# Kernel tuning notes

Measured on AMD Instinct MI355X. Metric: run time of the kernel, lower is better.

The kernel has to match this reference:

```python
import jax, jax.numpy as jnp
import numpy as np

JIT = 1e-4
LOG2PI = float(np.log(2.0 * np.pi))
BETA = 1e5
LOC_RADIUS = 5.0


def gaspari_cohn(radius, D):
    i = np.arange(D)
    dist = np.minimum(np.abs(i[:, None] - i[None, :]), D - np.abs(i[:, None] - i[None, :])).astype(np.float64)
    z = dist / radius
    zs = np.maximum(z, 1e-12)
    g1 = 1.0 - 5.0 / 3 * z**2 + 5.0 / 8 * z**3 + 0.5 * z**4 - 0.25 * z**5
    g2 = 4.0 - 5.0 * z + 5.0 / 3 * z**2 + 5.0 / 8 * z**3 - 0.5 * z**4 + 1.0 / 12 * z**5 - 2.0 / (3.0 * zs)
    return np.where(z < 1.0, g1, np.where(z < 2.0, g2, 0.0)).astype(np.float32)


def sq_dist(x, z):
    # x: [..., n, d], z: [..., m, d] (broadcastable)
    x2 = jnp.sum(x * x, -1)[..., :, None]
    z2 = jnp.sum(z * z, -1)[..., None, :]
    d2 = x2 + z2 - 2.0 * jnp.matmul(x, jnp.swapaxes(z, -1, -2))
    return jnp.maximum(d2, 0.0)


def setup_inputs():
    key = jax.random.key(0)
    ks = jax.random.split(key, 12)
    D, dy, M, N, B, T = 32, 32, 128, 128, 8, 48
    ips = jax.random.normal(ks[0], (D, M, D), dtype=jnp.float32)
    H = jnp.eye(dy, D, dtype=jnp.float32)
    lengthscale = jnp.full((D,), 2.0, dtype=jnp.float32)
    outputscale = jnp.ones((D,), dtype=jnp.float32)
    q_mu = 0.1 * jax.random.normal(ks[1], (D, M), dtype=jnp.float32)
    q_L = jnp.tril(0.02 * jax.random.normal(ks[2], (D, M, M), dtype=jnp.float32), -1) + 0.1 * jnp.eye(M, dtype=jnp.float32)[None]
    q_noise = jnp.full((D,), 0.05**2, dtype=jnp.float32)
    r_noise = jnp.full((dy,), 0.1**2, dtype=jnp.float32)
    x0 = jax.random.normal(ks[3], (N, D, B, D), dtype=jnp.float32)
    y = 0.5 * jax.random.normal(ks[4], (B, T, dy), dtype=jnp.float32)
    eps_u = jax.random.normal(ks[5], (N, D, M), dtype=jnp.float32)
    eps_f = jax.random.normal(ks[6], (T, N, D, B), dtype=jnp.float32)
    eps_q = jax.random.normal(ks[7], (T, B, N, D), dtype=jnp.float32)
    eps_r = jax.random.normal(ks[8], (T, B, N, dy), dtype=jnp.float32)
    return {"ips": ips, "H": H, "lengthscale": lengthscale, "outputscale": outputscale,
            "q_mu": q_mu, "q_L": q_L, "q_noise": q_noise, "r_noise": r_noise,
            "x0": x0, "y": y, "eps_u": eps_u, "eps_f": eps_f, "eps_q": eps_q, "eps_r": eps_r}


def _forward(ips, H, lengthscale, outputscale, q_mu, q_L, q_noise, r_noise, x0, y, eps_u, eps_f, eps_q, eps_r):
    N, D, B, _ = x0.shape
    M = ips.shape[1]
    dy = y.shape[-1]
    taper = jnp.asarray(gaspari_cohn(LOC_RADIUS, D))
    ls = lengthscale[:, None, None]
    osc = outputscale[:, None, None]
    zs = ips / ls  # [D, M, D]
    Kzz = osc * jnp.exp(-0.5 * sq_dist(zs, zs)) + JIT * jnp.eye(M, dtype=x0.dtype)  # [D,M,M]
    # U ~ q(u): consistent sampling of inducing outputs per ensemble member
    U = q_mu[None] + jnp.einsum('dmk,ndk->ndm', q_L, eps_u)                 # [N,D,M]
    A = jnp.linalg.solve(Kzz[None], U[..., None])[..., 0]                    # Kzz^{-1} u, [N,D,M]
    # KL(q(u) || N(0, Kzz)) summed over tasks
    Lzz = jnp.linalg.cholesky(Kzz)
    Sq = q_L @ jnp.swapaxes(q_L, -1, -2)
    trace = jnp.sum(jnp.diagonal(jnp.linalg.solve(Kzz, Sq), axis1=-2, axis2=-1))
    mah = jnp.sum(q_mu * jnp.linalg.solve(Kzz, q_mu[..., None])[..., 0])
    logdetK = 2.0 * jnp.sum(jnp.log(jnp.diagonal(Lzz, axis1=-2, axis2=-1)))
    logdetS = 2.0 * jnp.sum(jnp.log(jnp.abs(jnp.diagonal(q_L, axis1=-2, axis2=-1))))
    kl = 0.5 * (trace + mah - D * M + logdetK - logdetS)

    q_sd = jnp.sqrt(q_noise)
    r_sd = jnp.sqrt(r_noise)
    R = jnp.diag(r_noise)
    Ht = H.T
    eyeB = jnp.eye(B, dtype=x0.dtype)

    def step(carry, inp):
        x_prev, ll = carry
        y_t, ef, eq, er = inp
        # ---- GP prediction (conditioned on sampled U) ----
        xq = x_prev / lengthscale[None, :, None, None]                       # [N,D,B,D]
        Kxz = outputscale[None, :, None, None] * jnp.exp(-0.5 * sq_dist(xq, zs[None]))  # [N,D,B,M]
        Kxx = outputscale[None, :, None, None] * jnp.exp(-0.5 * sq_dist(xq, xq))        # [N,D,B,B]
        mean = jnp.einsum('ndbm,ndm->ndb', Kxz, A)
        V = jnp.linalg.solve(Kzz[None], jnp.swapaxes(Kxz, -1, -2))           # [N,D,M,B]
        cov = Kxx - jnp.matmul(Kxz, V) + JIT * eyeB
        Lc = jnp.linalg.cholesky(cov)
        f = mean + jnp.einsum('ndbc,ndc->ndb', Lc, ef)                       # rsample, [N,D,B]
        X = jnp.transpose(f, (2, 0, 1))                                      # [B,N,D]
        X = X + eq * q_sd                                                    # + chol(Q) noise
        Xm = jnp.mean(X, axis=-2, keepdims=True)                             # [B,1,D]
        Xc = X - Xm
        P = taper * (jnp.swapaxes(Xc, -1, -2) @ Xc) / (N - 1)                # localized cov [B,D,D]
        # ---- EnKF update ----
        S = H @ P @ Ht + R                                                   # [B,dy,dy]
        Ls = jnp.linalg.cholesky(S)
        resid = y_t - (Xm @ Ht)[:, 0]                                        # [B,dy]
        alpha = jnp.linalg.solve(S, resid[..., None])[..., 0]
        logdetS_t = 2.0 * jnp.sum(jnp.log(jnp.diagonal(Ls, axis1=-2, axis2=-1)), axis=-1)
        ll_t = -0.5 * jnp.sum(dy * LOG2PI + logdetS_t + jnp.sum(resid * alpha, -1))
        PHt = P @ Ht
        K = jnp.swapaxes(jnp.linalg.solve(S, jnp.swapaxes(PHt, -1, -2)), -1, -2)  # [B,D,dy]
        y_pert = y_t[:, None, :] + er * r_sd
        X_post = X + (y_pert - X @ Ht) @ jnp.swapaxes(K, -1, -2)
        Xm_post = jnp.mean(X_post, axis=-2)                                  # [B,D]
        P_post = P - K @ (H @ P)
        x_next = jnp.broadcast_to(Xm_post[None, None], (N, D, B, D))         # ensemble reset to post. mean
        return (x_next, ll + ll_t), (Xm_post, jnp.diagonal(P_post, axis1=-2, axis2=-1))

    ys = jnp.swapaxes(y, 0, 1)  # [T,B,dy]
    (x_final, ll), (fm, fv) = jax.lax.scan(step, (x0, jnp.asarray(0.0, x0.dtype)), (ys, eps_f, eps_q, eps_r))
    filtered_mean = jnp.swapaxes(fm, 0, 1)  # [B,T,D]
    filtered_var = jnp.swapaxes(fv, 0, 1)   # [B,T,D]
    elbo = ll - kl / BETA
    return elbo, x_final, filtered_mean, filtered_var


def reference(ips, H, lengthscale, outputscale, q_mu, q_L, q_noise, r_noise, x0, y, eps_u, eps_f, eps_q, eps_r):
    return _forward(ips, H, lengthscale, outputscale, q_mu, q_L, q_noise, r_noise, x0, y, eps_u, eps_f, eps_q, eps_r)
```

## Files before the change

### kernel.cpp

```cpp
#include <hip/hip_runtime.h>

#define JITF 1e-4f
#define LOG2PIF 1.8378770664093454f

#define WZSM   0
#define WZS2   131072
#define WKINV  135168
#define WA     659456
#define WXW    1708032
#define WXM    1740800
#define WLLB   1741056
#define WKLD   1741088
#define WCNT   1741248
#define OFM 1048577
#define OFV 1060865

__device__ __forceinline__ float dot4f(const float4 a, const float4 b) {
  return fmaf(a.x, b.x, fmaf(a.y, b.y, fmaf(a.z, b.z, a.w * b.w)));
}
__device__ __forceinline__ float4 f4_fma(const float4 a, const float s, const float4 c) {
  return make_float4(fmaf(a.x,s,c.x), fmaf(a.y,s,c.y), fmaf(a.z,s,c.z), fmaf(a.w,s,c.w));
}
__device__ __forceinline__ float4 f4_axpby(const float a, const float4 x, const float b, const float4 y) {
  return make_float4(fmaf(a,x.x,b*y.x), fmaf(a,x.y,b*y.y), fmaf(a,x.z,b*y.z), fmaf(a,x.w,b*y.w));
}
__device__ __forceinline__ float aloadf(const float* p) {
  return __hip_atomic_load((float*)p, __ATOMIC_RELAXED, __HIP_MEMORY_SCOPE_AGENT);
}
__device__ __forceinline__ void astoref(float* p, float v) {
  __hip_atomic_store(p, v, __ATOMIC_RELAXED, __HIP_MEMORY_SCOPE_AGENT);
}
__device__ __forceinline__ unsigned long long aloadu(const unsigned long long* p) {
  return __hip_atomic_load((unsigned long long*)p, __ATOMIC_RELAXED, __HIP_MEMORY_SCOPE_AGENT);
}
__device__ __forceinline__ void pollge(const int* p, int target) {
  while (__hip_atomic_load((int*)p, __ATOMIC_RELAXED, __HIP_MEMORY_SCOPE_AGENT) < target)
    __builtin_amdgcn_s_sleep(1);
}
__device__ __forceinline__ void gsignal(int* p, int val, int tid) {
  __syncthreads();
  if (tid == 0) __hip_atomic_store(p, val, __ATOMIC_RELEASE, __HIP_MEMORY_SCOPE_AGENT);
}

__global__ __launch_bounds__(1024) void k_sweep(
    const float* __restrict__ ips, const float* __restrict__ ls, const float* __restrict__ osc,
    const float* __restrict__ qL, const float* __restrict__ qmu,
    float* __restrict__ zsMg, float* __restrict__ zs2g,
    float* __restrict__ Kinvg, float* __restrict__ kld, int* cnt)
{
  __shared__ float sm[40200];
  float* cur   = sm;
  float* qLs   = sm + 16896;
  float* zsM   = sm + 33792;
  float* rowP0 = sm + 38400;
  float* rowP1 = sm + 38532;
  float* colP0 = sm + 38664;
  float* colP1 = sm + 38792;
  float* qms   = sm + 38920;
  float* zs2   = sm + 39048;
  float* red   = sm + 39176;
  float4* cur4 = (float4*)cur;
  const float4* zsM4 = (const float4*)zsM;
  float4* rowP04 = (float4*)rowP0;
  float4* rowP14 = (float4*)rowP1;
  const int d = blockIdx.x, tid = threadIdx.x;
  const float invl = 1.0f / ls[d], oscd = osc[d];

  if (blockIdx.x == 0) { for (int l = tid; l < 640; l += 1024) cnt[l] = 0; }

  for (int l = tid; l < 4096; l += 1024) {
    int m = l >> 5, k = l & 31;
    zsM[m*36+k] = ips[(d*128+m)*32+k] * invl;
  }
  for (int l = tid; l < 16384; l += 1024)
    qLs[(l>>7)*132 + (l&127)] = qL[d*16384 + l];
  if (tid < 128) qms[tid] = qmu[d*128+tid];
  __syncthreads();
  if (tid < 128) {
    float s = 0.f;
#pragma unroll
    for (int kq = 0; kq < 8; kq++) { float4 v = zsM4[tid*9+kq]; s += dot4f(v, v); }
    zs2[tid] = s; zs2g[d*128+tid] = s;
  }
  for (int l = tid; l < 4096; l += 1024) zsMg[d*4096+l] = zsM[(l>>5)*36 + (l&31)];
  __syncthreads();

  const int i = tid >> 3, q = tid & 7;
  {
    float4 zr[8];
#pragma unroll
    for (int kq = 0; kq < 8; kq++) zr[kq] = zsM4[i*9+kq];
    float z2i = zs2[i];
    for (int jj = 0; jj < 16; jj++) {
      int j = q*16 + jj;
      float dot = 0.f;
#pragma unroll
      for (int kq = 0; kq < 8; kq++) dot += dot4f(zr[kq], zsM4[j*9+kq]);
      float d2 = fmaxf(z2i + zs2[j] - 2.f*dot, 0.f);
      cur[i*132+j] = oscd * expf(-0.5f*d2) + (i == j ? JITF : 0.f);
    }
  }
  __syncthreads();

  float llog = 0.f;
#pragma unroll 1
  for (int kb = 0; kb < 64; kb++) {
    const int k0 = 2*kb, k1 = k0+1;
    if (tid < 33) rowP04[tid] = cur4[k0*33 + tid];
    else if (tid < 66) rowP14[tid-33] = cur4[k1*33 + (tid-33)];
    else if (tid < 194) colP0[tid-66] = cur[(tid-66)*132 + k0];
    else if (tid < 322) colP1[tid-194] = cur[(tid-194)*132 + k1];
    __syncthreads();
    const float a  = rowP0[k0];
    const float bb = rowP0[k1];
    const float c  = rowP1[k1];
    const float det = fmaf(a, c, -bb*bb);
    const float idet = 1.0f/det;
    if (tid == 0) llog += logf(det);
    const float ci0 = colP0[i], ci1 = colP1[i];
    const float w0 = (ci0*c - ci1*bb)*idet;
    const float w1 = (ci1*a - ci0*bb)*idet;
    const bool isk0 = (i == k0), isk1 = (i == k1);
    const int jqp = k0 >> 2;
    const int c0 = k0 & 3;
    auto body = [&](int jq) {
      float4 r0 = rowP04[jq];
      float4 r1 = rowP14[jq];
      float4 nv;
      if (isk0)      nv = f4_axpby(c*idet, r0, -bb*idet, r1);
      else if (isk1) nv = f4_axpby(-bb*idet, r0, a*idet, r1);
      else {
        nv = cur4[i*33+jq];
        nv = f4_fma(r0, -w0, nv);
        nv = f4_fma(r1, -w1, nv);
      }
      if (jq == jqp) {
        float pv0, pv1;
        if (isk0)      { pv0 = -c*idet;  pv1 =  bb*idet; }
        else if (isk1) { pv0 =  bb*idet; pv1 = -a*idet;  }
        else           { pv0 =  w0;      pv1 =  w1;      }
        if (c0 == 0) { nv.x = pv0; nv.y = pv1; }
        else         { nv.z = pv0; nv.w = pv1; }
      }
      cur4[i*33+jq] = nv;
    };
#pragma unroll
    for (int jj = 0; jj < 4; jj++) body(q*4 + jj);
    if (q == 7) body(32);
    __syncthreads();
  }
  for (int e = tid; e < 16384; e += 1024) { int ii = e>>7, jj = e&127; cur[ii*132+jj] = -cur[ii*132+jj]; }
  __syncthreads();
  for (int l = tid; l < 4096; l += 1024) ((float4*)(Kinvg + d*16384))[l] = cur4[(l>>5)*33 + (l&31)];

  if (tid == 0) kld[d] = 0.5f * llog;
  red[tid] = (tid < 128) ? logf(fabsf(qLs[tid*132+tid])) : 0.f;
  __syncthreads();
  for (int s = 512; s > 0; s >>= 1) { if (tid < s) red[tid] += red[tid+s]; __syncthreads(); }
  if (tid == 0) kld[96+d] = red[0];
  __syncthreads();
  {
    float macc = 0.f;
    for (int e = tid; e < 16384; e += 1024) {
      int ii = e >> 7, jj = e & 127;
      macc = fmaf(cur[ii*132+jj], qms[ii]*qms[jj], macc);
    }
    red[tid] = macc;
    __syncthreads();
    for (int s = 512; s > 0; s >>= 1) { if (tid < s) red[tid] += red[tid+s]; __syncthreads(); }
    if (tid == 0) kld[64+d] = red[0];
    __syncthreads();
  }
  {
    float tacc = 0.f;
    for (int e = tid; e < 16384; e += 1024) {
      int ii = e >> 7, k2 = e & 127;
      if (k2 <= ii) {
        float w = 0.f;
        for (int m = k2; m < 128; m++) w = fmaf(cur[ii*132+m], qLs[m*132+k2], w);
        tacc = fmaf(w, qLs[ii*132+k2], tacc);
      }
    }
    red[tid] = tacc;
    __syncthreads();
    for (int s = 512; s > 0; s >>= 1) { if (tid < s) red[tid] += red[tid+s]; __syncthreads(); }
    if (tid == 0) kld[32+d] = red[0];
  }
}

__global__ __launch_bounds__(256) void k_UA(
    const float* __restrict__ qL, const float* __restrict__ qmu, const float* __restrict__ eu,
    const float* __restrict__ Kinv, float* __restrict__ A)
{
  __shared__ float big[16512];
  __shared__ float Us[4128];
  __shared__ float eus[4128];
  const int d = blockIdx.x >> 2, nc = blockIdx.x & 3, tid = threadIdx.x;
  const int n0 = nc * 32;
  for (int l = tid; l < 16384; l += 256) big[(l>>7)*129 + (l&127)] = qL[d*16384 + l];
  for (int l = tid; l < 4096; l += 256)
    eus[(l>>7)*129 + (l&127)] = eu[((n0 + (l>>7))*32 + d)*128 + (l&127)];
  __syncthreads();
  for (int e = tid; e < 4096; e += 256) {
    int nl = e >> 7, m = e & 127;
    float s0 = qmu[d*128 + m], s1 = 0.f, s2 = 0.f, s3 = 0.f;
    int kmax = m + 1, k4 = kmax & ~3, k = 0;
    for (; k < k4; k += 4) {
      s0 = fmaf(big[m*129+k],   eus[nl*129+k],   s0);
      s1 = fmaf(big[m*129+k+1], eus[nl*129+k+1], s1);
      s2 = fmaf(big[m*129+k+2], eus[nl*129+k+2], s2);
      s3 = fmaf(big[m*129+k+3], eus[nl*129+k+3], s3);
    }
    for (; k < kmax; k++) s0 = fmaf(big[m*129+k], eus[nl*129+k], s0);
    Us[nl*129+m] = (s0+s1)+(s2+s3);
  }
  __syncthreads();
  for (int l = tid; l < 16384; l += 256) big[(l>>7)*129 + (l&127)] = Kinv[d*16384 + l];
  __syncthreads();
  for (int e = tid; e < 4096; e += 256) {
    int nl = e >> 7, m = e & 127;
    float s0 = 0.f, s1 = 0.f, s2 = 0.f, s3 = 0.f;
    for (int k = 0; k < 128; k += 4) {
      s0 = fmaf(big[m*129+k],   Us[nl*129+k],   s0);
      s1 = fmaf(big[m*129+k+1], Us[nl*129+k+1], s1);
      s2 = fmaf(big[m*129+k+2], Us[nl*129+k+2], s2);
      s3 = fmaf(big[m*129+k+3], Us[nl*129+k+3], s3);
    }
    A[((n0+nl)*32 + d)*128 + m] = (s0+s1)+(s2+s3);
  }
}

__global__ __launch_bounds__(128) void k_t0gp(
    const float* __restrict__ x0, const float* __restrict__ ls, const float* __restrict__ osc,
    const float* __restrict__ qn, const float* __restrict__ zsMg, const float* __restrict__ zs2g,
    const float* __restrict__ Kinv, const float* __restrict__ A,
    const float* __restrict__ ef, const float* __restrict__ eq, float* __restrict__ Xw)
{
  __shared__ float xqs[8*36];
  __shared__ float xq2s[8];
  __shared__ float Kxzs[8*132];
  __shared__ float T1s[8*132];
  __shared__ float covs[8][9];
  __shared__ float Lc[8][9];
  __shared__ float Arow[132];
  const float4* xqs4  = (const float4*)xqs;
  const float4* Kxzs4 = (const float4*)Kxzs;
  const float4* T1s4  = (const float4*)T1s;
  const float4* Arow4 = (const float4*)Arow;
  const int n = blockIdx.x >> 5, d = blockIdx.x & 31, tid = threadIdx.x;
  const float invl = 1.0f / ls[d], oscd = osc[d];

  float4 zr[8];
  {
    const float4* zrow = (const float4*)(zsMg + d*4096 + tid*32);
#pragma unroll
    for (int kq = 0; kq < 8; kq++) zr[kq] = zrow[kq];
  }
  const float z2m = zs2g[d*128 + tid];
  for (int l = tid; l < 256; l += 128) {
    int b = l >> 5, k = l & 31;
    xqs[b*36+k] = x0[((n*32+d)*8 + b)*32 + k] * invl;
  }
  Arow[tid] = A[(n*32+d)*128 + tid];
  __syncthreads();
  if (tid < 8) {
    float s = 0.f;
#pragma unroll
    for (int kq = 0; kq < 8; kq++) { float4 v = xqs4[tid*9+kq]; s += dot4f(v, v); }
    xq2s[tid] = s;
  }
  __syncthreads();
  {
#pragma unroll
    for (int b = 0; b < 8; b++) {
      float dot = 0.f;
#pragma unroll
      for (int kq = 0; kq < 8; kq++) dot += dot4f(zr[kq], xqs4[b*9+kq]);
      Kxzs[b*132+tid] = oscd * expf(-0.5f * fmaxf(xq2s[b] + z2m - 2.f*dot, 0.f));
    }
  }
  __syncthreads();
  {
    float a[8] = {0.f,0.f,0.f,0.f,0.f,0.f,0.f,0.f};
    const float* kp = Kinv + d*16384 + tid;
    for (int mq = 0; mq < 32; mq++) {
      float kv0 = kp[(4*mq+0)*128];
      float kv1 = kp[(4*mq+1)*128];
      float kv2 = kp[(4*mq+2)*128];
      float kv3 = kp[(4*mq+3)*128];
#pragma unroll
      for (int b = 0; b < 8; b++) {
        float4 kx = Kxzs4[b*33+mq];
        a[b] = fmaf(kx.x, kv0, fmaf(kx.y, kv1, fmaf(kx.z, kv2, fmaf(kx.w, kv3, a[b]))));
      }
    }
#pragma unroll
    for (int b = 0; b < 8; b++) T1s[b*132+tid] = a[b];
  }
  __syncthreads();
  if (tid < 64) {
    int b = tid >> 3, c = tid & 7;
    float sc = 0.f, dt = 0.f;
#pragma unroll
    for (int mq = 0; mq < 32; mq++) sc += dot4f(T1s4[b*33+mq], Kxzs4[c*33+mq]);
#pragma unroll
    for (int kq = 0; kq < 8; kq++) dt += dot4f(xqs4[b*9+kq], xqs4[c*9+kq]);
    float kxx = oscd * expf(-0.5f * fmaxf(xq2s[b] + xq2s[c] - 2.f*dt, 0.f));
    covs[b][c] = kxx - sc + (b == c ? JITF : 0.f);
  }
  __syncthreads();
  if (tid == 0) {
    for (int a = 0; a < 8; a++) {
      float s = covs[a][a];
      for (int k = 0; k < a; k++) s -= Lc[a][k]*Lc[a][k];
      float la = sqrtf(s);
      Lc[a][a] = la;
      for (int i2 = a+1; i2 < 8; i2++) {
        float s2 = covs[i2][a];
        for (int k = 0; k < a; k++) s2 -= Lc[i2][k]*Lc[a][k];
        Lc[i2][a] = s2 / la;
      }
    }
  }
  __syncthreads();
  if (tid < 8) {
    int b = tid;
    float mv = 0.f;
#pragma unroll
    for (int mq = 0; mq < 32; mq++) mv += dot4f(Kxzs4[b*33+mq], Arow4[mq]);
    float f = mv;
#pragma unroll
    for (int c = 0; c < 8; c++) if (c <= b) f = fmaf(Lc[b][c], ef[(n*32+d)*8 + c], f);
    float X = f + eq[(b*128+n)*32 + d] * sqrtf(qn[d]);
    Xw[(d*8+b)*128 + n] = X;
  }
}

__global__ __launch_bounds__(1024) void k_scan(
    const float* __restrict__ ls, const float* __restrict__ osc,
    const float* __restrict__ qn, const float* __restrict__ rn,
    const float* __restrict__ y,
    const float* __restrict__ ef, const float* __restrict__ eq, const float* __restrict__ er,
    const float* __restrict__ zsMg, const float* __restrict__ zs2g,
    const float* __restrict__ Kinvg, const float* __restrict__ Ag,
    float* Xw, float* xm, float* llb, const float* __restrict__ kld,
    float* out, int* cnt)
{
  __shared__ float sm[36704];
  const int blk = blockIdx.x, tid = threadIdx.x;

  if (blk < 32) {
    const int d = blk;
    float* KinvS = sm;
    float* AT    = sm + 16512;
    float* KxzS  = sm + 33024;
    float* T1S   = sm + 34080;
    float* xqS   = sm + 35136;
    float* efS   = sm + 35424;
    float* covS  = sm + 36576;
    const float invl = 1.0f/ls[d], oscd = osc[d], qsd = sqrtf(qn[d]);
    const float4* KxzS4 = (const float4*)KxzS;
    const float4* T1S4  = (const float4*)T1S;
    const float4* xqS4  = (const float4*)xqS;
    const unsigned long long* xm_u = (const unsigned long long*)xm;

    for (int l = tid; l < 16384; l += 1024)
      KinvS[(l>>7)*129 + (l&127)] = Kinvg[d*16384 + l];
    for (int l = tid; l < 16384; l += 1024) {
      int n = l >> 7, m = l & 127;
      AT[m*129 + n] = Ag[(n*32 + d)*128 + m];
    }

    const int bb = tid >> 7, mn = tid & 127;
    float4 zr[8];
    {
      const float4* zrow = (const float4*)(zsMg + d*4096 + mn*32);
#pragma unroll
      for (int kq = 0; kq < 8; kq++) zr[kq] = zrow[kq];
    }
    const float z2m = zs2g[d*128 + mn];
    __syncthreads();

    for (int t = 1; t < 48; t++) {
      const float v_ef = ef[((t*128 + (tid>>3))*32 + d)*8 + (tid&7)];
      const float v_eq = eq[((t*8+bb)*128 + mn)*32 + d];

      if (tid < 8) pollge(cnt + (32+tid)*16, t);
      __syncthreads();
      if (tid < 128) {
        unsigned long long u = aloadu(xm_u + tid);
        float2 f = __builtin_bit_cast(float2, u);
        int b2 = tid >> 4, k2 = (tid & 15)*2;
        xqS[b2*36 + k2]     = f.x * invl;
        xqS[b2*36 + k2 + 1] = f.y * invl;
      }
      efS[(tid>>3)*9 + (tid&7)] = v_ef;
      __syncthreads();
      {
        float dot = 0.f, sq = 0.f;
#pragma unroll
        for (int kq = 0; kq < 8; kq++) {
          float4 x4 = xqS4[bb*9+kq];
          dot += dot4f(zr[kq], x4);
          sq  += dot4f(x4, x4);
        }
        KxzS[bb*132+mn] = oscd * expf(-0.5f * fmaxf(sq + z2m - 2.f*dot, 0.f));
      }
      __syncthreads();
      float mv;
      {
        float t1a = 0.f, t1b = 0.f, ma = 0.f, mb2 = 0.f;
#pragma unroll 8
        for (int mm = 0; mm < 128; mm += 2) {
          float kx0 = KxzS[bb*132+mm], kx1 = KxzS[bb*132+mm+1];
          t1a = fmaf(kx0, KinvS[mm*129+mn],     t1a);
          t1b = fmaf(kx1, KinvS[(mm+1)*129+mn], t1b);
          ma  = fmaf(kx0, AT[mm*129+mn],        ma);
          mb2 = fmaf(kx1, AT[(mm+1)*129+mn],    mb2);
        }
        T1S[bb*132+mn] = t1a + t1b;
        mv = ma + mb2;
      }
      __syncthreads();
      if (tid < 64) {
        int b = tid >> 3, c = tid & 7;
        float sc = 0.f, dt = 0.f, sqb = 0.f, sqc = 0.f;
#pragma unroll
        for (int mq = 0; mq < 32; mq++) sc += dot4f(T1S4[b*33+mq], KxzS4[c*33+mq]);
#pragma unroll
        for (int kq = 0; kq < 8; kq++) {
          float4 xb = xqS4[b*9+kq], xc = xqS4[c*9+kq];
          dt += dot4f(xb, xc); sqb += dot4f(xb, xb); sqc += dot4f(xc, xc);
        }
        float kxx = oscd*expf(-0.5f*fmaxf(sqb + sqc - 2.f*dt, 0.f));
        covS[b*9+c] = kxx - sc + (b==c ? JITF : 0.f);
      }
      __syncthreads();
      {
        float Lc[8][8];
        float f = mv;
#pragma unroll
        for (int a = 0; a < 8; a++) {
          float s = covS[a*9+a];
#pragma unroll
          for (int k = 0; k < 8; k++) if (k < a) s -= Lc[a][k]*Lc[a][k];
          float la = sqrtf(s);
          Lc[a][a] = la;
          if (a == bb) f = fmaf(la, efS[mn*9+a], f);
          float ila = 1.0f / la;
#pragma unroll
          for (int i2 = 0; i2 < 8; i2++) if (i2 > a) {
            float s2 = covS[i2*9+a];
#pragma unroll
            for (int k = 0; k < 8; k++) if (k < a) s2 -= Lc[i2][k]*Lc[a][k];
            float lv = s2 * ila;
            Lc[i2][a] = lv;
            if (i2 == bb) f = fmaf(lv, efS[mn*9+a], f);
          }
        }
        f = fmaf(v_eq, qsd, f);
        astoref(Xw + (d*8+bb)*128 + mn, f);
      }
      gsignal(cnt + d*16, t, tid);
    }
    if (tid < 8) pollge(cnt + (32+tid)*16, 48);
    __syncthreads();
  } else {
    const int b = blk - 32;
    float* XN     = sm;
    float* Ps     = sm + 4224;
    float* Sinvs  = sm + 5376;
    float* taperS = sm + 6432;
    float* mersS  = sm + 7456;
    float* rowP   = sm + 8992;
    float* colP   = sm + 9136;
    float* detS   = sm + 9280;
    float* XmsS   = sm + 9296;
    float* residS = sm + 9328;
    float* miS    = sm + 9360;
    float* rsdS   = sm + 9392;
    float* rnS    = sm + 9424;
    const float4* er4 = (const float4*)er;
    const unsigned long long* Xw_u = (const unsigned long long*)Xw;

    if (tid < 1024) {
      int ii = tid >> 5, jj = tid & 31;
      int ad = ii - jj; if (ad < 0) ad = -ad;
      int dist = (ad < 32 - ad) ? ad : (32 - ad);
      double z = (double)dist / 5.0;
      double z2 = z*z, z3 = z2*z, z4 = z3*z, z5 = z4*z;
      double gval;
      if (z < 1.0) gval = 1.0 - (5.0/3.0)*z2 + (5.0/8.0)*z3 + 0.5*z4 - 0.25*z5;
      else if (z < 2.0) gval = 4.0 - 5.0*z + (5.0/3.0)*z2 + (5.0/8.0)*z3 - 0.5*z4 + (1.0/12.0)*z5 - 2.0/(3.0*z);
      else gval = 0.0;
      taperS[tid] = (float)gval;
    }
    if (tid < 32) { rnS[tid] = rn[tid]; rsdS[tid] = sqrtf(rn[tid]); }
    if (tid < 384) {
      int tt = tid >> 3, jq = tid & 7;
      float sx = 0.f, sy = 0.f, sz = 0.f, sw = 0.f;
      for (int n = 0; n < 128; n++) {
        float4 e = er4[((tt*8+b)*128+n)*8 + jq];
        sx += e.x; sy += e.y; sz += e.z; sw += e.w;
      }
      int o = tt*32 + jq*4;
      mersS[o]   = sx*(1.f/128.f);
      mersS[o+1] = sy*(1.f/128.f);
      mersS[o+2] = sz*(1.f/128.f);
      mersS[o+3] = sw*(1.f/128.f);
    }
    __syncthreads();

    float llacc = 0.f;
    const int i = tid >> 5, j = tid & 31;
    for (int t = 0; t < 48; t++) {
      float yv = 0.f;
      if (tid < 32) yv = y[(b*48+t)*32 + tid];
      if (t > 0) { if (tid < 32) pollge(cnt + tid*16, t); }
      __syncthreads();
      {
        unsigned long long u0 = aloadu(Xw_u + (i*8+b)*64 + j);
        unsigned long long u1 = aloadu(Xw_u + (i*8+b)*64 + j + 32);
        float2 f0 = __builtin_bit_cast(float2, u0);
        float2 f1 = __builtin_bit_cast(float2, u1);
        float s4 = (f0.x+f0.y)+(f1.x+f1.y);
#pragma unroll
        for (int mk = 1; mk <= 16; mk <<= 1) s4 += __shfl_xor(s4, mk, 64);
        float mu = s4 * (1.f/128.f);
        if (j == 0) XmsS[i] = mu;
        XN[(2*j)*33+i]    = f0.x - mu;
        XN[(2*j+1)*33+i]  = f0.y - mu;
        XN[(2*j+64)*33+i] = f1.x - mu;
        XN[(2*j+65)*33+i] = f1.y - mu;
      }
      __syncthreads();
      float val;
      {
        float a0 = 0.f, a1 = 0.f;
#pragma unroll 4
        for (int n = 0; n < 128; n += 2) {
          a0 = fmaf(XN[n*33+i],     XN[n*33+j],     a0);
          a1 = fmaf(XN[(n+1)*33+i], XN[(n+1)*33+j], a1);
        }
        float pv = taperS[i*32+j] * (a0+a1) * (1.f/127.f);
        Ps[i*36+j] = pv;
        val = pv + ((i==j) ? rnS[i] : 0.f);
      }
#pragma unroll 1
      for (int kb = 0; kb < 16; kb++) {
        int k0 = kb*2, k1 = k0+1, par = (kb&1)*72;
        if (i == k0) rowP[par + j]      = val;
        if (i == k1) rowP[par + 36 + j] = val;
        if (j == k0) colP[par + i]      = val;
        if (j == k1) colP[par + 36 + i] = val;
        __syncthreads();
        float a  = rowP[par + k0];
        float bb = rowP[par + k1];
        float c  = rowP[par + 36 + k1];
        float det = fmaf(a, c, -bb*bb);
        float idet = 1.0f/det;
        float ci0 = colP[par + i], ci1 = colP[par + 36 + i];
        float r0j = rowP[par + j], r1j = rowP[par + 36 + j];
        float w0 = (ci0*c - ci1*bb)*idet;
        float w1 = (ci1*a - ci0*bb)*idet;
        float v0 = (c*r0j - bb*r1j)*idet;
        float v1 = (a*r1j - bb*r0j)*idet;
        float nv = val - w0*r0j - w1*r1j;
        if (i == k0) nv = v0;
        if (i == k1) nv = v1;
        if (j == k0) nv = w0;
        if (j == k1) nv = w1;
        if (i == k0 && j == k0) nv = -c*idet;
        if (i == k0 && j == k1) nv =  bb*idet;
        if (i == k1 && j == k0) nv =  bb*idet;
        if (i == k1 && j == k1) nv = -a*idet;
        val = nv;
        if (tid == 0) detS[kb] = det;
      }
      Sinvs[i*33+j] = -val;
      if (tid < 32) {
        float rs = yv - XmsS[tid];
        residS[tid] = rs;
        miS[tid] = fmaf(mersS[t*32+tid], rsdS[tid], rs);
      }
      __syncthreads();
      if (tid < 32) {
        float bt = 0.f;
#pragma unroll
        for (int k = 0; k < 32; k++) bt = fmaf(Sinvs[tid*33+k], miS[k], bt);
        float xmp = XmsS[tid] + miS[tid] - rnS[tid]*bt;
        out[OFM + (b*48+t)*32 + tid] = xmp;
        out[OFV + (b*48+t)*32 + tid] = rnS[tid] - rnS[tid]*rnS[tid]*Sinvs[tid*33+tid];
        astoref(xm + b*32 + tid, xmp);
      } else if (tid < 64) {
        int ii = tid - 32;
        float al = 0.f;
#pragma unroll
        for (int k = 0; k < 32; k++) al = fmaf(Sinvs[ii*33+k], residS[k], al);
        float contrib = al * residS[ii] + ((ii < 16) ? logf(detS[ii]) : 0.f);
#pragma unroll
        for (int mk = 1; mk <= 16; mk <<= 1) contrib += __shfl_xor(contrib, mk, 64);
        if (ii == 0) {
          llacc += -0.5f*(32.f*LOG2PIF + contrib);
          if (t == 47) astoref(llb + b, llacc);
        }
      }
      gsignal(cnt + (32+b)*16, t+1, tid);
    }
    if (tid < 8) pollge(cnt + (32+tid)*16, 48);
    __syncthreads();
  }

  if (tid < 128) {
    unsigned long long u = aloadu((const unsigned long long*)xm + tid);
    float2 f = __builtin_bit_cast(float2, u);
    sm[2*tid] = f.x; sm[2*tid+1] = f.y;
  }
  __syncthreads();
  for (int v = blk*1024 + tid; v < 1048576; v += 40960)
    out[1 + v] = sm[v & 255];
  if (blk == 32 && tid == 0) {
    double ll = 0.0;
    for (int i2 = 0; i2 < 8; i2++) ll += (double)aloadf(llb + i2);
    double ldK = 0.0, tr = 0.0, mah = 0.0, ldS = 0.0;
    for (int d2 = 0; d2 < 32; d2++) {
      ldK += (double)kld[d2];
      tr  += (double)kld[32+d2];
      mah += (double)kld[64+d2];
      ldS += (double)kld[96+d2];
    }
    double klv = 0.5*(tr + mah - 4096.0 + 2.0*ldK - 2.0*ldS);
    out[0] = (float)(ll - klv/100000.0);
  }
}

extern "C" void kernel_launch(void* const* d_in, const int* in_sizes, int n_in,
                              void* d_out, int out_size, void* d_ws, size_t ws_size,
                              hipStream_t stream) {
  const float* ips = (const float*)d_in[0];
  const float* ls  = (const float*)d_in[2];
  const float* osc = (const float*)d_in[3];
  const float* qmu = (const float*)d_in[4];
  const float* qL  = (const float*)d_in[5];
  const float* qn  = (const float*)d_in[6];
  const float* rn  = (const float*)d_in[7];
  const float* x0  = (const float*)d_in[8];
  const float* y   = (const float*)d_in[9];
  const float* eu  = (const float*)d_in[10];
  const float* ef  = (const float*)d_in[11];
  const float* eq  = (const float*)d_in[12];
  const float* er  = (const float*)d_in[13];
  float* out = (float*)d_out;
  float* ws  = (float*)d_ws;

  float* w_zsm  = ws + WZSM;
  float* w_zs2  = ws + WZS2;
  float* w_kinv = ws + WKINV;
  float* w_A    = ws + WA;
  float* w_Xw   = ws + WXW;
  float* w_xm   = ws + WXM;
  float* w_llb  = ws + WLLB;
  float* w_kld  = ws + WKLD;
  int*   w_cnt  = (int*)(ws + WCNT);

  k_sweep<<<32, 1024, 0, stream>>>(ips, ls, osc, qL, qmu, w_zsm, w_zs2, w_kinv, w_kld, w_cnt);
  k_UA<<<128, 256, 0, stream>>>(qL, qmu, eu, w_kinv, w_A);
  k_t0gp<<<4096, 128, 0, stream>>>(x0, ls, osc, qn, w_zsm, w_zs2, w_kinv, w_A, ef, eq, w_Xw);
  void* args[] = { (void*)&ls, (void*)&osc, (void*)&qn, (void*)&rn, (void*)&y,
                   (void*)&ef, (void*)&eq, (void*)&er, (void*)&w_zsm, (void*)&w_zs2,
                   (void*)&w_kinv, (void*)&w_A, (void*)&w_Xw, (void*)&w_xm, (void*)&w_llb,
                   (void*)&w_kld, (void*)&out, (void*)&w_cnt };
  hipLaunchCooperativeKernel((void*)k_scan, dim3(40), dim3(1024), args, 0, stream);
}
```

Baseline: 1.625 ms.

## Replace counter barriers with tagged per-element handoff and 4x4 block Gauss-Jordan sweep

Producer/consumer blocks in the cooperative scan now exchange data through 64-bit words that pack the value with a timestep tag. Consumers spin on each element's tag, which removes the separate counter signal, its extra __syncthreads, and the release/acquire round trip per step. The in-block 32x32 sweep inversion also now pivots on 4x4 blocks instead of 2x2, so it needs 8 barrier-separated iterations instead of 16. In exchange each element poll is a wider atomic load that may spin, the workspace layout changes, and the larger pivot blocks add arithmetic and possible numerical differences.

```diff
diff --git a/kernel.cpp b/kernel.cpp
--- a/kernel.cpp
+++ b/kernel.cpp
@@ -2,16 +2,18 @@
 
 #define JITF 1e-4f
 #define LOG2PIF 1.8378770664093454f
+
+typedef unsigned long long ull;
 
 #define WZSM   0
 #define WZS2   131072
 #define WKINV  135168
 #define WA     659456
-#define WXW    1708032
-#define WXM    1740800
-#define WLLB   1741056
-#define WKLD   1741088
-#define WCNT   1741248
+#define WXWT   1183744
+#define WXMT   1249280
+#define WLLB   1249792
+#define WKLD   1249824
+#define WCNT   1249984
 #define OFM 1048577
 #define OFV 1060865
 
@@ -30,16 +32,23 @@
 __device__ __forceinline__ void astoref(float* p, float v) {
   __hip_atomic_store(p, v, __ATOMIC_RELAXED, __HIP_MEMORY_SCOPE_AGENT);
 }
-__device__ __forceinline__ unsigned long long aloadu(const unsigned long long* p) {
-  return __hip_atomic_load((unsigned long long*)p, __ATOMIC_RELAXED, __HIP_MEMORY_SCOPE_AGENT);
+__device__ __forceinline__ void astoreu(ull* p, ull v) {
+  __hip_atomic_store(p, v, __ATOMIC_RELAXED, __HIP_MEMORY_SCOPE_AGENT);
+}
+__device__ __forceinline__ ull packft(float f, int tag) {
+  return (ull)__float_as_uint(f) | ((ull)(unsigned)tag << 32);
+}
+__device__ __forceinline__ float pollft(const ull* p, int tag) {
+  ull u = __hip_atomic_load((ull*)p, __ATOMIC_RELAXED, __HIP_MEMORY_SCOPE_AGENT);
+  while ((int)(u >> 32) != tag) {
+    __builtin_amdgcn_s_sleep(1);
+    u = __hip_atomic_load((ull*)p, __ATOMIC_RELAXED, __HIP_MEMORY_SCOPE_AGENT);
+  }
+  return __uint_as_float((unsigned)u);
 }
 __device__ __forceinline__ void pollge(const int* p, int target) {
   while (__hip_atomic_load((int*)p, __ATOMIC_RELAXED, __HIP_MEMORY_SCOPE_AGENT) < target)
     __builtin_amdgcn_s_sleep(1);
-}
-__device__ __forceinline__ void gsignal(int* p, int val, int tid) {
-  __syncthreads();
-  if (tid == 0) __hip_atomic_store(p, val, __ATOMIC_RELEASE, __HIP_MEMORY_SCOPE_AGENT);
 }
 
 __global__ __launch_bounds__(1024) void k_sweep(
@@ -234,7 +243,7 @@
     const float* __restrict__ x0, const float* __restrict__ ls, const float* __restrict__ osc,
     const float* __restrict__ qn, const float* __restrict__ zsMg, const float* __restrict__ zs2g,
     const float* __restrict__ Kinv, const float* __restrict__ A,
-    const float* __restrict__ ef, const float* __restrict__ eq, float* __restrict__ Xw)
+    const float* __restrict__ ef, const float* __restrict__ eq, ull* __restrict__ XwT)
 {
   __shared__ float xqs[8*36];
   __shared__ float xq2s[8];
@@ -332,7 +341,7 @@
 #pragma unroll
     for (int c = 0; c < 8; c++) if (c <= b) f = fmaf(Lc[b][c], ef[(n*32+d)*8 + c], f);
     float X = f + eq[(b*128+n)*32 + d] * sqrtf(qn[d]);
-    Xw[(d*8+b)*128 + n] = X;
+    astoreu(XwT + (d*8+b)*128 + n, packft(X, 0));
   }
 }
 
@@ -343,7 +352,7 @@
     const float* __restrict__ ef, const float* __restrict__ eq, const float* __restrict__ er,
     const float* __restrict__ zsMg, const float* __restrict__ zs2g,
     const float* __restrict__ Kinvg, const float* __restrict__ Ag,
-    float* Xw, float* xm, float* llb, const float* __restrict__ kld,
+    ull* XwT, ull* xmT, float* llb, const float* __restrict__ kld,
     float* out, int* cnt)
 {
   __shared__ float sm[36704];
@@ -362,7 +371,6 @@
     const float4* KxzS4 = (const float4*)KxzS;
     const float4* T1S4  = (const float4*)T1S;
     const float4* xqS4  = (const float4*)xqS;
-    const unsigned long long* xm_u = (const unsigned long long*)xm;
 
     for (int l = tid; l < 16384; l += 1024)
       KinvS[(l>>7)*129 + (l&127)] = Kinvg[d*16384 + l];
@@ -385,14 +393,9 @@
       const float v_ef = ef[((t*128 + (tid>>3))*32 + d)*8 + (tid&7)];
       const float v_eq = eq[((t*8+bb)*128 + mn)*32 + d];
 
-      if (tid < 8) pollge(cnt + (32+tid)*16, t);
-      __syncthreads();
-      if (tid < 128) {
-        unsigned long long u = aloadu(xm_u + tid);
-        float2 f = __builtin_bit_cast(float2, u);
-        int b2 = tid >> 4, k2 = (tid & 15)*2;
-        xqS[b2*36 + k2]     = f.x * invl;
-        xqS[b2*36 + k2 + 1] = f.y * invl;
+      if (tid < 256) {
+        float v = pollft(xmT + tid, t-1);
+        xqS[(tid>>5)*36 + (tid&31)] = v * invl;
       }
       efS[(tid>>3)*9 + (tid&7)] = v_ef;
       __syncthreads();
@@ -459,12 +462,10 @@
           }
         }
         f = fmaf(v_eq, qsd, f);
-        astoref(Xw + (d*8+bb)*128 + mn, f);
-      }
-      gsignal(cnt + d*16, t, tid);
-    }
-    if (tid < 8) pollge(cnt + (32+tid)*16, 48);
-    __syncthreads();
+        astoreu(XwT + (d*8+bb)*128 + mn, packft(f, t));
+      }
+      __syncthreads();
+    }
   } else {
     const int b = blk - 32;
     float* XN     = sm;
@@ -473,15 +474,14 @@
     float* taperS = sm + 6432;
     float* mersS  = sm + 7456;
     float* rowP   = sm + 8992;
-    float* colP   = sm + 9136;
-    float* detS   = sm + 9280;
-    float* XmsS   = sm + 9296;
-    float* residS = sm + 9328;
-    float* miS    = sm + 9360;
-    float* rsdS   = sm + 9392;
-    float* rnS    = sm + 9424;
+    float* colP   = sm + 9280;
+    float* detS   = sm + 9568;
+    float* XmsS   = sm + 9576;
+    float* residS = sm + 9608;
+    float* miS    = sm + 9640;
+    float* rsdS   = sm + 9672;
+    float* rnS    = sm + 9704;
     const float4* er4 = (const float4*)er;
-    const unsigned long long* Xw_u = (const unsigned long long*)Xw;
 
     if (tid < 1024) {
       int ii = tid >> 5, jj = tid & 31;
@@ -516,22 +516,21 @@
     for (int t = 0; t < 48; t++) {
       float yv = 0.f;
       if (tid < 32) yv = y[(b*48+t)*32 + tid];
-      if (t > 0) { if (tid < 32) pollge(cnt + tid*16, t); }
-      __syncthreads();
       {
-        unsigned long long u0 = aloadu(Xw_u + (i*8+b)*64 + j);
-        unsigned long long u1 = aloadu(Xw_u + (i*8+b)*64 + j + 32);
-        float2 f0 = __builtin_bit_cast(float2, u0);
-        float2 f1 = __builtin_bit_cast(float2, u1);
-        float s4 = (f0.x+f0.y)+(f1.x+f1.y);
+        const ull* base = XwT + (i*8+b)*128;
+        float x0v = pollft(base + 2*j,      t);
+        float x1v = pollft(base + 2*j + 1,  t);
+        float x2v = pollft(base + 2*j + 64, t);
+        float x3v = pollft(base + 2*j + 65, t);
+        float s4 = (x0v+x1v)+(x2v+x3v);
 #pragma unroll
         for (int mk = 1; mk <= 16; mk <<= 1) s4 += __shfl_xor(s4, mk, 64);
         float mu = s4 * (1.f/128.f);
         if (j == 0) XmsS[i] = mu;
-        XN[(2*j)*33+i]    = f0.x - mu;
-        XN[(2*j+1)*33+i]  = f0.y - mu;
-        XN[(2*j+64)*33+i] = f1.x - mu;
-        XN[(2*j+65)*33+i] = f1.y - mu;
+        XN[(2*j)*33+i]    = x0v - mu;
+        XN[(2*j+1)*33+i]  = x1v - mu;
+        XN[(2*j+64)*33+i] = x2v - mu;
+        XN[(2*j+65)*33+i] = x3v - mu;
       }
       __syncthreads();
       float val;
@@ -547,35 +546,67 @@
         val = pv + ((i==j) ? rnS[i] : 0.f);
       }
 #pragma unroll 1
-      for (int kb = 0; kb < 16; kb++) {
-        int k0 = kb*2, k1 = k0+1, par = (kb&1)*72;
-        if (i == k0) rowP[par + j]      = val;
-        if (i == k1) rowP[par + 36 + j] = val;
-        if (j == k0) colP[par + i]      = val;
-        if (j == k1) colP[par + 36 + i] = val;
+      for (int kb = 0; kb < 8; kb++) {
+        const int k0 = kb*4;
+        float* rowPb = rowP + (kb&1)*144;
+        float* colPb = colP + (kb&1)*144;
+        if (i >= k0 && i < k0+4) rowPb[(i-k0)*36 + j] = val;
+        if (j >= k0 && j < k0+4) colPb[(j-k0)*36 + i] = val;
         __syncthreads();
-        float a  = rowP[par + k0];
-        float bb = rowP[par + k1];
-        float c  = rowP[par + 36 + k1];
-        float det = fmaf(a, c, -bb*bb);
-        float idet = 1.0f/det;
-        float ci0 = colP[par + i], ci1 = colP[par + 36 + i];
-        float r0j = rowP[par + j], r1j = rowP[par + 36 + j];
-        float w0 = (ci0*c - ci1*bb)*idet;
-        float w1 = (ci1*a - ci0*bb)*idet;
-        float v0 = (c*r0j - bb*r1j)*idet;
-        float v1 = (a*r1j - bb*r0j)*idet;
-        float nv = val - w0*r0j - w1*r1j;
-        if (i == k0) nv = v0;
-        if (i == k1) nv = v1;
-        if (j == k0) nv = w0;
-        if (j == k1) nv = w1;
-        if (i == k0 && j == k0) nv = -c*idet;
-        if (i == k0 && j == k1) nv =  bb*idet;
-        if (i == k1 && j == k0) nv =  bb*idet;
-        if (i == k1 && j == k1) nv = -a*idet;
+        float p00 = rowPb[0*36+k0+0], p01 = rowPb[0*36+k0+1], p02 = rowPb[0*36+k0+2], p03 = rowPb[0*36+k0+3];
+        float p11 = rowPb[1*36+k0+1], p12 = rowPb[1*36+k0+2], p13 = rowPb[1*36+k0+3];
+        float p22 = rowPb[2*36+k0+2], p23 = rowPb[2*36+k0+3], p33 = rowPb[3*36+k0+3];
+        float deta = fmaf(p00, p11, -p01*p01);
+        float ia = 1.0f/deta;
+        float ai00 = p11*ia, ai01 = -p01*ia, ai11 = p00*ia;
+        float m00 = ai00*p02 + ai01*p12;
+        float m01 = ai00*p03 + ai01*p13;
+        float m10 = ai01*p02 + ai11*p12;
+        float m11 = ai01*p03 + ai11*p13;
+        float s00 = p22 - (p02*m00 + p12*m10);
+        float s01 = p23 - (p02*m01 + p12*m11);
+        float s11 = p33 - (p03*m01 + p13*m11);
+        float dets = fmaf(s00, s11, -s01*s01);
+        float is = 1.0f/dets;
+        float si00 = s11*is, si01 = -s01*is, si11 = s00*is;
+        float n00 = m00*si00 + m01*si01;
+        float n01 = m00*si01 + m01*si11;
+        float n10 = m10*si00 + m11*si01;
+        float n11 = m10*si01 + m11*si11;
+        float q00 = ai00 + n00*m00 + n01*m01;
+        float q01 = ai01 + n00*m10 + n01*m11;
+        float q11 = ai11 + n10*m10 + n11*m11;
+        const float PI[4][4] = {
+          {  q00,  q01, -n00, -n01 },
+          {  q01,  q11, -n10, -n11 },
+          { -n00, -n10, si00, si01 },
+          { -n01, -n11, si01, si11 }
+        };
+        if (tid == 0) detS[kb] = deta * dets;
+        float cI[4], rJ[4];
+#pragma unroll
+        for (int a = 0; a < 4; a++) { cI[a] = colPb[a*36 + i]; rJ[a] = rowPb[a*36 + j]; }
+        float w[4];
+#pragma unroll
+        for (int bq = 0; bq < 4; bq++)
+          w[bq] = cI[0]*PI[0][bq] + cI[1]*PI[1][bq] + cI[2]*PI[2][bq] + cI[3]*PI[3][bq];
+        float interior = val - (w[0]*rJ[0] + w[1]*rJ[1] + w[2]*rJ[2] + w[3]*rJ[3]);
+        const int r = i - k0, c = j - k0;
+        const bool ip = (r >= 0 && r < 4), jp = (c >= 0 && c < 4);
+        float pr[4], pc[4];
+#pragma unroll
+        for (int bq = 0; bq < 4; bq++) {
+          pr[bq] = (r==0) ? PI[0][bq] : (r==1) ? PI[1][bq] : (r==2) ? PI[2][bq] : PI[3][bq];
+          pc[bq] = (c==0) ? PI[bq][0] : (c==1) ? PI[bq][1] : (c==2) ? PI[bq][2] : PI[bq][3];
+        }
+        float rowv = pr[0]*rJ[0] + pr[1]*rJ[1] + pr[2]*rJ[2] + pr[3]*rJ[3];
+        float colv = cI[0]*pc[0] + cI[1]*pc[1] + cI[2]*pc[2] + cI[3]*pc[3];
+        float prc  = (c==0) ? pr[0] : (c==1) ? pr[1] : (c==2) ? pr[2] : pr[3];
+        float nv = interior;
+        if (ip) nv = rowv;
+        if (jp) nv = colv;
+        if (ip && jp) nv = -prc;
         val = nv;
-        if (tid == 0) detS[kb] = det;
       }
       Sinvs[i*33+j] = -val;
       if (tid < 32) {
@@ -591,13 +622,13 @@
         float xmp = XmsS[tid] + miS[tid] - rnS[tid]*bt;
         out[OFM + (b*48+t)*32 + tid] = xmp;
         out[OFV + (b*48+t)*32 + tid] = rnS[tid] - rnS[tid]*rnS[tid]*Sinvs[tid*33+tid];
-        astoref(xm + b*32 + tid, xmp);
+        astoreu(xmT + b*32 + tid, packft(xmp, t));
       } else if (tid < 64) {
         int ii = tid - 32;
         float al = 0.f;
 #pragma unroll
         for (int k = 0; k < 32; k++) al = fmaf(Sinvs[ii*33+k], residS[k], al);
-        float contrib = al * residS[ii] + ((ii < 16) ? logf(detS[ii]) : 0.f);
+        float contrib = al * residS[ii] + ((ii < 8) ? logf(detS[ii]) : 0.f);
 #pragma unroll
         for (int mk = 1; mk <= 16; mk <<= 1) contrib += __shfl_xor(contrib, mk, 64);
         if (ii == 0) {
@@ -605,21 +636,18 @@
           if (t == 47) astoref(llb + b, llacc);
         }
       }
-      gsignal(cnt + (32+b)*16, t+1, tid);
-    }
-    if (tid < 8) pollge(cnt + (32+tid)*16, 48);
-    __syncthreads();
-  }
-
-  if (tid < 128) {
-    unsigned long long u = aloadu((const unsigned long long*)xm + tid);
-    float2 f = __builtin_bit_cast(float2, u);
-    sm[2*tid] = f.x; sm[2*tid+1] = f.y;
-  }
+      __syncthreads();
+    }
+    if (tid == 0)
+      __hip_atomic_store(cnt + (32+b)*16, 1, __ATOMIC_RELEASE, __HIP_MEMORY_SCOPE_AGENT);
+  }
+
+  if (tid < 256) sm[tid] = pollft(xmT + tid, 47);
   __syncthreads();
   for (int v = blk*1024 + tid; v < 1048576; v += 40960)
     out[1 + v] = sm[v & 255];
   if (blk == 32 && tid == 0) {
+    for (int b2 = 0; b2 < 8; b2++) pollge(cnt + (32+b2)*16, 1);
     double ll = 0.0;
     for (int i2 = 0; i2 < 8; i2++) ll += (double)aloadf(llb + i2);
     double ldK = 0.0, tr = 0.0, mah = 0.0, ldS = 0.0;
@@ -657,18 +685,18 @@
   float* w_zs2  = ws + WZS2;
   float* w_kinv = ws + WKINV;
   float* w_A    = ws + WA;
-  float* w_Xw   = ws + WXW;
-  float* w_xm   = ws + WXM;
+  ull*   w_xwt  = (ull*)(ws + WXWT);
+  ull*   w_xmt  = (ull*)(ws + WXMT);
   float* w_llb  = ws + WLLB;
   float* w_kld  = ws + WKLD;
   int*   w_cnt  = (int*)(ws + WCNT);
 
   k_sweep<<<32, 1024, 0, stream>>>(ips, ls, osc, qL, qmu, w_zsm, w_zs2, w_kinv, w_kld, w_cnt);
   k_UA<<<128, 256, 0, stream>>>(qL, qmu, eu, w_kinv, w_A);
-  k_t0gp<<<4096, 128, 0, stream>>>(x0, ls, osc, qn, w_zsm, w_zs2, w_kinv, w_A, ef, eq, w_Xw);
+  k_t0gp<<<4096, 128, 0, stream>>>(x0, ls, osc, qn, w_zsm, w_zs2, w_kinv, w_A, ef, eq, w_xwt);
   void* args[] = { (void*)&ls, (void*)&osc, (void*)&qn, (void*)&rn, (void*)&y,
                    (void*)&ef, (void*)&eq, (void*)&er, (void*)&w_zsm, (void*)&w_zs2,
-                   (void*)&w_kinv, (void*)&w_A, (void*)&w_Xw, (void*)&w_xm, (void*)&w_llb,
+                   (void*)&w_kinv, (void*)&w_A, (void*)&w_xwt, (void*)&w_xmt, (void*)&w_llb,
                    (void*)&w_kld, (void*)&out, (void*)&w_cnt };
   hipLaunchCooperativeKernel((void*)k_scan, dim3(40), dim3(1024), args, 0, stream);
 }
```

New measurement: 1.885 ms. 16.0% more time.
